# Kernel tuning notes

Hardware: AMD Instinct MI355X
Metric: run time of the kernel (lower is better)

## Reference

```python
import jax, jax.numpy as jnp
import numpy as np

Q = 1  # hidden size is hardcoded to 1 in the module's forward


def lcg_zscore(m, n):
    """Deterministic LCG weight generator used by RADAM's ELM, z-scored."""
    L = m * n
    if L == 1:
        return np.ones((1, 1), dtype=np.float32)
    V = np.zeros(L, dtype=np.float64)
    V[0] = L + 1
    a, b, c = L + 2, L + 3, float(L) * float(L)
    for i in range(1, L):
        V[i] = (a * V[i - 1] + b) % c
    V = (V - V.mean()) / V.std()
    return V.reshape(m, n).astype(np.float32)


def setup_inputs() -> dict:
    key = jax.random.key(0)
    B, Z, W, H = 32, 2048, 32, 32
    x = jax.random.normal(key, (B, Z, W, H), dtype=jnp.float32)
    alpha = jnp.asarray(lcg_zscore(Q, Z))  # (Q, z) fixed random encoder weights
    return {"x": x, "alpha": alpha}


def reference(x, alpha):
    # Batched ELM-autoencoder fit replacing the per-sample Python loop.
    B, Z, W, H = x.shape
    N = W * H
    X = x.reshape(B, Z, N)  # feature_map per sample: (z, w*h)
    # hidden activations H = sigmoid(alpha @ X): (B, Q, N)
    Hact = jax.nn.sigmoid(jnp.einsum('qz,bzn->bqn', alpha, X))
    # ELM-AE output weights beta = pinv(H^T) @ X^T, shape (B, Q, z).
    # For Q=1 H^T is an N x 1 full-column-rank matrix (sigmoid > 0), so
    # pinv(H^T) = H / ||H||^2 exactly -- closed form, no SVD needed.
    denom = jnp.sum(Hact * Hact, axis=-1, keepdims=True)  # (B, Q, 1)
    beta = jnp.einsum('bqn,bzn->bqz', Hact, X) / denom     # (B, Q, z)
    return beta.reshape(B, Q * Z, 1)
```

## Files before the change

kernel.cpp:

```cpp
#include <hip/hip_runtime.h>
#include <math.h>

constexpr int BB   = 32;
constexpr int ZD   = 2048;
constexpr int ND   = 1024;
constexpr int ZC   = 32;
constexpr int ZPC  = ZD / ZC;

using f32x4 = __attribute__((ext_vector_type(4))) float;

__global__ __launch_bounds__(256) void k1_partial(const float* __restrict__ x,
                                                  const float* __restrict__ alpha,
                                                  float* __restrict__ partial) {
    const int blk = blockIdx.x;
    const int b   = blk >> 5;
    const int c   = blk & (ZC - 1);
    const int t   = threadIdx.x;
    const f32x4* x4 = (const f32x4*)x + ((size_t)(b * ZD + c * ZPC)) * (ND / 4) + t;
    const float* al = alpha + c * ZPC;
    f32x4 acc = {0.f, 0.f, 0.f, 0.f};
#pragma unroll 8
    for (int z = 0; z < ZPC; ++z) {
        const float a = al[z];
        const f32x4 v = x4[(size_t)z * (ND / 4)];
        acc.x = fmaf(a, v.x, acc.x);
        acc.y = fmaf(a, v.y, acc.y);
        acc.z = fmaf(a, v.z, acc.z);
        acc.w = fmaf(a, v.w, acc.w);
    }
    __builtin_nontemporal_store(acc, (f32x4*)partial + (size_t)blk * (ND / 4) + t);
}

__global__ __launch_bounds__(1024) void k2_finalize(const float* __restrict__ partial,
                                                    float* __restrict__ hd) {
    const int b = blockIdx.x;
    const int n = threadIdx.x;
    float s = 0.f;
#pragma unroll
    for (int c = 0; c < ZC; ++c)
        s += __builtin_nontemporal_load(partial + ((size_t)(b * ZC + c)) * ND + n);
    const float hv = 1.0f / (1.0f + expf(-s));

    float d = hv * hv;
#pragma unroll
    for (int o = 32; o > 0; o >>= 1) d += __shfl_down(d, o);
    __shared__ float red[16];
    __shared__ float tot_s;
    const int lane = n & 63, w = n >> 6;
    if (lane == 0) red[w] = d;
    __syncthreads();
    if (n == 0) {
        float tot = 0.f;
#pragma unroll
        for (int i = 0; i < 16; ++i) tot += red[i];
        tot_s = tot;
    }
    __syncthreads();
    hd[b * ND + n] = hv / tot_s;
}

__global__ __launch_bounds__(256) void k3_beta(const float* __restrict__ x,
                                               const float* __restrict__ hd,
                                               float* __restrict__ out) {
    const int blk = blockIdx.x;
    const int b   = (BB - 1) - (blk >> 7);
    const int zb  = (blk & 127) * 16;
    const int t    = threadIdx.x;
    const int wave = t >> 6;
    const int lane = t & 63;

    const f32x4* h4 = (const f32x4*)(hd + (size_t)b * ND);
    const f32x4 h0 = h4[lane];
    const f32x4 h1 = h4[lane + 64];
    const f32x4 h2 = h4[lane + 128];
    const f32x4 h3 = h4[lane + 192];

    const f32x4* base = (const f32x4*)(x + ((size_t)(b * ZD + zb + wave * 4)) * ND);
    float s0, s1, s2, s3;
    {
        const f32x4 a0 = __builtin_nontemporal_load(base + lane);
        const f32x4 a1 = __builtin_nontemporal_load(base + lane + 64);
        const f32x4 a2 = __builtin_nontemporal_load(base + lane + 128);
        const f32x4 a3 = __builtin_nontemporal_load(base + lane + 192);
        s0 = a0.x*h0.x + a0.y*h0.y + a0.z*h0.z + a0.w*h0.w
           + a1.x*h1.x + a1.y*h1.y + a1.z*h1.z + a1.w*h1.w
           + a2.x*h2.x + a2.y*h2.y + a2.z*h2.z + a2.w*h2.w
           + a3.x*h3.x + a3.y*h3.y + a3.z*h3.z + a3.w*h3.w;
    }
    {
        const f32x4* row = base + (ND / 4);
        const f32x4 a0 = __builtin_nontemporal_load(row + lane);
        const f32x4 a1 = __builtin_nontemporal_load(row + lane + 64);
        const f32x4 a2 = __builtin_nontemporal_load(row + lane + 128);
        const f32x4 a3 = __builtin_nontemporal_load(row + lane + 192);
        s1 = a0.x*h0.x + a0.y*h0.y + a0.z*h0.z + a0.w*h0.w
           + a1.x*h1.x + a1.y*h1.y + a1.z*h1.z + a1.w*h1.w
           + a2.x*h2.x + a2.y*h2.y + a2.z*h2.z + a2.w*h2.w
           + a3.x*h3.x + a3.y*h3.y + a3.z*h3.z + a3.w*h3.w;
    }
    {
        const f32x4* row = base + 2 * (ND / 4);
        const f32x4 a0 = __builtin_nontemporal_load(row + lane);
        const f32x4 a1 = __builtin_nontemporal_load(row + lane + 64);
        const f32x4 a2 = __builtin_nontemporal_load(row + lane + 128);
        const f32x4 a3 = __builtin_nontemporal_load(row + lane + 192);
        s2 = a0.x*h0.x + a0.y*h0.y + a0.z*h0.z + a0.w*h0.w
           + a1.x*h1.x + a1.y*h1.y + a1.z*h1.z + a1.w*h1.w
           + a2.x*h2.x + a2.y*h2.y + a2.z*h2.z + a2.w*h2.w
           + a3.x*h3.x + a3.y*h3.y + a3.z*h3.z + a3.w*h3.w;
    }
    {
        const f32x4* row = base + 3 * (ND / 4);
        const f32x4 a0 = __builtin_nontemporal_load(row + lane);
        const f32x4 a1 = __builtin_nontemporal_load(row + lane + 64);
        const f32x4 a2 = __builtin_nontemporal_load(row + lane + 128);
        const f32x4 a3 = __builtin_nontemporal_load(row + lane + 192);
        s3 = a0.x*h0.x + a0.y*h0.y + a0.z*h0.z + a0.w*h0.w
           + a1.x*h1.x + a1.y*h1.y + a1.z*h1.z + a1.w*h1.w
           + a2.x*h2.x + a2.y*h2.y + a2.z*h2.z + a2.w*h2.w
           + a3.x*h3.x + a3.y*h3.y + a3.z*h3.z + a3.w*h3.w;
    }
#pragma unroll
    for (int o = 32; o > 0; o >>= 1) {
        s0 += __shfl_down(s0, o);
        s1 += __shfl_down(s1, o);
        s2 += __shfl_down(s2, o);
        s3 += __shfl_down(s3, o);
    }
    if (lane == 0) {
        float* o = out + b * ZD + zb + wave * 4;
        o[0] = s0; o[1] = s1; o[2] = s2; o[3] = s3;
    }
}

extern "C" void kernel_launch(void* const* d_in, const int* in_sizes, int n_in,
                              void* d_out, int out_size, void* d_ws, size_t ws_size,
                              hipStream_t stream) {
    const float* x     = (const float*)d_in[0];
    const float* alpha = (const float*)d_in[1];
    float* out = (float*)d_out;

    float* partial = (float*)d_ws;
    float* hd      = partial + (size_t)BB * ZC * ND;

    k1_partial<<<BB * ZC, 256, 0, stream>>>(x, alpha, partial);
    k2_finalize<<<BB, 1024, 0, stream>>>(partial, hd);
    k3_beta<<<BB * (ZD / 16), 256, 0, stream>>>(x, hd, out);
}
```

Before: 397.6 us.

## Fuse finalize into partial kernel via last-block atomic counter

```diff
diff --git a/kernel.cpp b/kernel.cpp
--- a/kernel.cpp
+++ b/kernel.cpp
@@ -9,9 +9,11 @@
 
 using f32x4 = __attribute__((ext_vector_type(4))) float;
 
-__global__ __launch_bounds__(256) void k1_partial(const float* __restrict__ x,
-                                                  const float* __restrict__ alpha,
-                                                  float* __restrict__ partial) {
+__global__ __launch_bounds__(256) void k1_partial_finalize(const float* __restrict__ x,
+                                                           const float* __restrict__ alpha,
+                                                           float* __restrict__ partial,
+                                                           float* __restrict__ hd,
+                                                           int* __restrict__ counters) {
     const int blk = blockIdx.x;
     const int b   = blk >> 5;
     const int c   = blk & (ZC - 1);
@@ -28,35 +30,41 @@
         acc.z = fmaf(a, v.z, acc.z);
         acc.w = fmaf(a, v.w, acc.w);
     }
-    __builtin_nontemporal_store(acc, (f32x4*)partial + (size_t)blk * (ND / 4) + t);
-}
+    ((f32x4*)partial)[(size_t)blk * (ND / 4) + t] = acc;
 
-__global__ __launch_bounds__(1024) void k2_finalize(const float* __restrict__ partial,
-                                                    float* __restrict__ hd) {
-    const int b = blockIdx.x;
-    const int n = threadIdx.x;
-    float s = 0.f;
+    __threadfence();
+    __shared__ int is_last;
+    if (t == 0)
+        is_last = (atomicAdd(&counters[b], 1) == ZC - 1) ? 1 : 0;
+    __syncthreads();
+    if (!is_last) return;
+    __threadfence();
+
+    float hv[4];
+    float d = 0.f;
 #pragma unroll
-    for (int c = 0; c < ZC; ++c)
-        s += __builtin_nontemporal_load(partial + ((size_t)(b * ZC + c)) * ND + n);
-    const float hv = 1.0f / (1.0f + expf(-s));
-
-    float d = hv * hv;
+    for (int j = 0; j < 4; ++j) {
+        const int n = t + 256 * j;
+        float s = 0.f;
+#pragma unroll
+        for (int cc = 0; cc < ZC; ++cc)
+            s += partial[((size_t)(b * ZC + cc)) * ND + n];
+        hv[j] = 1.0f / (1.0f + expf(-s));
+        d += hv[j] * hv[j];
+    }
 #pragma unroll
     for (int o = 32; o > 0; o >>= 1) d += __shfl_down(d, o);
-    __shared__ float red[16];
+    __shared__ float red[4];
     __shared__ float tot_s;
-    const int lane = n & 63, w = n >> 6;
+    const int lane = t & 63, w = t >> 6;
     if (lane == 0) red[w] = d;
     __syncthreads();
-    if (n == 0) {
-        float tot = 0.f;
+    if (t == 0) tot_s = red[0] + red[1] + red[2] + red[3];
+    __syncthreads();
+    const float inv = 1.0f / tot_s;
 #pragma unroll
-        for (int i = 0; i < 16; ++i) tot += red[i];
-        tot_s = tot;
-    }
-    __syncthreads();
-    hd[b * ND + n] = hv / tot_s;
+    for (int j = 0; j < 4; ++j)
+        hd[b * ND + t + 256 * j] = hv[j] * inv;
 }
 
 __global__ __launch_bounds__(256) void k3_beta(const float* __restrict__ x,
@@ -78,10 +86,8 @@
     const f32x4* base = (const f32x4*)(x + ((size_t)(b * ZD + zb + wave * 4)) * ND);
     float s0, s1, s2, s3;
     {
-        const f32x4 a0 = __builtin_nontemporal_load(base + lane);
-        const f32x4 a1 = __builtin_nontemporal_load(base + lane + 64);
-        const f32x4 a2 = __builtin_nontemporal_load(base + lane + 128);
-        const f32x4 a3 = __builtin_nontemporal_load(base + lane + 192);
+        const f32x4 a0 = base[lane],       a1 = base[lane + 64];
+        const f32x4 a2 = base[lane + 128], a3 = base[lane + 192];
         s0 = a0.x*h0.x + a0.y*h0.y + a0.z*h0.z + a0.w*h0.w
            + a1.x*h1.x + a1.y*h1.y + a1.z*h1.z + a1.w*h1.w
            + a2.x*h2.x + a2.y*h2.y + a2.z*h2.z + a2.w*h2.w
@@ -89,10 +95,8 @@
     }
     {
         const f32x4* row = base + (ND / 4);
-        const f32x4 a0 = __builtin_nontemporal_load(row + lane);
-        const f32x4 a1 = __builtin_nontemporal_load(row + lane + 64);
-        const f32x4 a2 = __builtin_nontemporal_load(row + lane + 128);
-        const f32x4 a3 = __builtin_nontemporal_load(row + lane + 192);
+        const f32x4 a0 = row[lane],       a1 = row[lane + 64];
+        const f32x4 a2 = row[lane + 128], a3 = row[lane + 192];
         s1 = a0.x*h0.x + a0.y*h0.y + a0.z*h0.z + a0.w*h0.w
            + a1.x*h1.x + a1.y*h1.y + a1.z*h1.z + a1.w*h1.w
            + a2.x*h2.x + a2.y*h2.y + a2.z*h2.z + a2.w*h2.w
@@ -100,10 +104,8 @@
     }
     {
         const f32x4* row = base + 2 * (ND / 4);
-        const f32x4 a0 = __builtin_nontemporal_load(row + lane);
-        const f32x4 a1 = __builtin_nontemporal_load(row + lane + 64);
-        const f32x4 a2 = __builtin_nontemporal_load(row + lane + 128);
-        const f32x4 a3 = __builtin_nontemporal_load(row + lane + 192);
+        const f32x4 a0 = row[lane],       a1 = row[lane + 64];
+        const f32x4 a2 = row[lane + 128], a3 = row[lane + 192];
         s2 = a0.x*h0.x + a0.y*h0.y + a0.z*h0.z + a0.w*h0.w
            + a1.x*h1.x + a1.y*h1.y + a1.z*h1.z + a1.w*h1.w
            + a2.x*h2.x + a2.y*h2.y + a2.z*h2.z + a2.w*h2.w
@@ -111,10 +113,8 @@
     }
     {
         const f32x4* row = base + 3 * (ND / 4);
-        const f32x4 a0 = __builtin_nontemporal_load(row + lane);
-        const f32x4 a1 = __builtin_nontemporal_load(row + lane + 64);
-        const f32x4 a2 = __builtin_nontemporal_load(row + lane + 128);
-        const f32x4 a3 = __builtin_nontemporal_load(row + lane + 192);
+        const f32x4 a0 = row[lane],       a1 = row[lane + 64];
+        const f32x4 a2 = row[lane + 128], a3 = row[lane + 192];
         s3 = a0.x*h0.x + a0.y*h0.y + a0.z*h0.z + a0.w*h0.w
            + a1.x*h1.x + a1.y*h1.y + a1.z*h1.z + a1.w*h1.w
            + a2.x*h2.x + a2.y*h2.y + a2.z*h2.z + a2.w*h2.w
@@ -142,8 +142,9 @@
 
     float* partial = (float*)d_ws;
     float* hd      = partial + (size_t)BB * ZC * ND;
+    int*   counters = (int*)(hd + (size_t)BB * ND);
 
-    k1_partial<<<BB * ZC, 256, 0, stream>>>(x, alpha, partial);
-    k2_finalize<<<BB, 1024, 0, stream>>>(partial, hd);
+    hipMemsetAsync(counters, 0, BB * sizeof(int), stream);
+    k1_partial_finalize<<<BB * ZC, 256, 0, stream>>>(x, alpha, partial, hd, counters);
     k3_beta<<<BB * (ZD / 16), 256, 0, stream>>>(x, hd, out);
 }
```

New measurement: 601.3 us. +51.3%, slower.
